# Kernel tuning notes

Hardware: AMD Instinct MI355X
Metric: run time of the kernel (lower is better)

The kernel has to match this reference:

```python
import jax, jax.numpy as jnp
import numpy as np
import math

B, S, D = 2, 2048, 2048
H, KV = 16, 4
HD = D // H          # 128
REP = H // KV        # 4


def setup_inputs() -> dict:
    key = jax.random.key(0)
    ks = jax.random.split(key, 6)
    x = jax.random.normal(ks[0], (B, S, D), dtype=jnp.float32)
    wq = jax.random.normal(ks[1], (D, D), dtype=jnp.float32) * (D ** -0.5)
    wk = jax.random.normal(ks[2], (KV * HD, D), dtype=jnp.float32) * (D ** -0.5)
    wv = jax.random.normal(ks[3], (KV * HD, D), dtype=jnp.float32) * (D ** -0.5)
    wo = jax.random.normal(ks[4], (D, D), dtype=jnp.float32) * (D ** -0.5)
    # RoPE frequencies: theta_i = 10000^(-2i/hd), angle = pos * theta_i
    inv_freq = 1.0 / (10000.0 ** (np.arange(0, HD, 2, dtype=np.float32) / HD))
    angles = np.arange(S, dtype=np.float32)[:, None] * inv_freq[None, :]  # [S, HD/2]
    freqs_cos = jnp.asarray(np.cos(angles), dtype=jnp.float32)
    freqs_sin = jnp.asarray(np.sin(angles), dtype=jnp.float32)
    return {"x": x, "wq": wq, "wk": wk, "wv": wv, "wo": wo,
            "freqs_cos": freqs_cos, "freqs_sin": freqs_sin}


def _rope(t, cos, sin):
    # t: [B, S, h, HD]; cos/sin: [S, HD/2]; complex multiply on (even, odd) pairs
    tr = t.reshape(*t.shape[:-1], HD // 2, 2)
    t0, t1 = tr[..., 0], tr[..., 1]
    c = cos[None, :, None, :]
    s = sin[None, :, None, :]
    o0 = t0 * c - t1 * s
    o1 = t0 * s + t1 * c
    return jnp.stack([o0, o1], axis=-1).reshape(t.shape)


def reference(x, wq, wk, wv, wo, freqs_cos, freqs_sin):
    # projections (torch Linear: y = x @ W.T)
    q = jnp.einsum('bsd,ed->bse', x, wq).reshape(B, S, H, HD)
    k = jnp.einsum('bsd,ed->bse', x, wk).reshape(B, S, KV, HD)
    v = jnp.einsum('bsd,ed->bse', x, wv).reshape(B, S, KV, HD)
    q = _rope(q, freqs_cos, freqs_sin)
    k = _rope(k, freqs_cos, freqs_sin)
    # GQA: repeat each kv head REP times -> [B, S, H, HD]
    k = jnp.repeat(k, REP, axis=2)
    v = jnp.repeat(v, REP, axis=2)
    # [B, H, S, HD]
    q = q.transpose(0, 2, 1, 3)
    k = k.transpose(0, 2, 1, 3)
    v = v.transpose(0, 2, 1, 3)
    scores = jnp.einsum('bhqd,bhkd->bhqk', q, k) * (1.0 / math.sqrt(HD))
    # faithful to torch: tril then masked_fill(scores == 0, -inf)
    scores = jnp.tril(scores)
    scores = jnp.where(scores == 0.0, -jnp.inf, scores)
    attn = jax.nn.softmax(scores, axis=-1)
    out = jnp.einsum('bhqk,bhkd->bhqd', attn, v)
    out = out.transpose(0, 2, 1, 3).reshape(B, S, D)
    return jnp.einsum('bsd,ed->bse', out, wo)
```

## Files before the change

kernel.cpp:

```cpp
#include <hip/hip_runtime.h>
#include <stdint.h>

#define B_ 2
#define S_ 2048
#define D_ 2048
#define NH 16
#define NKV 4
#define HD_ 128

typedef unsigned short u16;
typedef unsigned int u32;
typedef __attribute__((ext_vector_type(8))) __bf16 bf16x8;
typedef __attribute__((ext_vector_type(4))) float f32x4;
typedef __attribute__((ext_vector_type(16))) float f32x16;
typedef __attribute__((ext_vector_type(4))) unsigned int u32x4;
typedef __attribute__((ext_vector_type(8))) unsigned short ushort8v;

__device__ __forceinline__ u16 f2bf(float f) {
  u32 u = __builtin_bit_cast(u32, f);
  u32 r = (u + 0x7FFFu + ((u >> 16) & 1u)) >> 16;
  return (u16)r;
}
__device__ __forceinline__ float bf2f(u16 h) {
  return __builtin_bit_cast(float, ((u32)h) << 16);
}
__device__ __forceinline__ u32 cvtpk(float lo, float hi) {
  u32 r;
  asm("v_cvt_pk_bf16_f32 %0, %1, %2" : "=v"(r) : "v"(lo), "v"(hi));
  return r;
}
__device__ __forceinline__ f32x16 zero16() {
  f32x16 v;
#pragma unroll
  for (int i = 0; i < 16; ++i) v[i] = 0.f;
  return v;
}

__device__ __forceinline__ void gld_lds16(const void* g, void* l) {
  __builtin_amdgcn_global_load_lds(
      (const __attribute__((address_space(1))) void*)g,
      (__attribute__((address_space(3))) void*)l, 16, 0, 0);
}

__device__ __forceinline__ void cv8(const float* s, u16* d, int i) {
  const float4* sp = (const float4*)s + 2 * (size_t)i;
  float4 a = sp[0], b = sp[1];
  ushort8v o;
  o[0] = f2bf(a.x); o[1] = f2bf(a.y); o[2] = f2bf(a.z); o[3] = f2bf(a.w);
  o[4] = f2bf(b.x); o[5] = f2bf(b.y); o[6] = f2bf(b.z); o[7] = f2bf(b.w);
  *((ushort8v*)d + i) = o;
}
__global__ __launch_bounds__(256) void k_f2b_all(const float* __restrict__ x,
    const float* __restrict__ wq, const float* __restrict__ wk,
    const float* __restrict__ wv, const float* __restrict__ wo,
    u16* __restrict__ xb, u16* __restrict__ wqkv, u16* __restrict__ wob) {
  int i = blockIdx.x * 256 + threadIdx.x;
  if (i < 1048576) { cv8(x, xb, i); return; }
  i -= 1048576;
  if (i < 524288) { cv8(wq, wqkv, i); return; }
  i -= 524288;
  if (i < 131072) { cv8(wk, wqkv + 2048 * 2048, i); return; }
  i -= 131072;
  if (i < 131072) { cv8(wv, wqkv + 2560 * 2048, i); return; }
  i -= 131072;
  if (i < 524288) cv8(wo, wob, i);
}

__global__ __launch_bounds__(256) void k_gemm_bf(const u16* __restrict__ A,
    const u16* __restrict__ W, u16* __restrict__ C, int N, int K) {
  __shared__ char lds[32768];
  char* ldsA = lds;
  char* ldsB = lds + 16384;
  const int tid = threadIdx.x;
  const int lane = tid & 63;
  const int wave = tid >> 6;
  const int m0 = blockIdx.x * 128, n0 = blockIdx.y * 128;
  const int wm = (wave >> 1) * 64, wn = (wave & 1) * 64;
  f32x4 acc[4][4];
#pragma unroll
  for (int i = 0; i < 4; ++i)
#pragma unroll
    for (int j = 0; j < 4; ++j) acc[i][j] = f32x4{0.f, 0.f, 0.f, 0.f};
  const size_t Kb2 = (size_t)K * 2;
  int rowS[4], colS[4];
#pragma unroll
  for (int j = 0; j < 4; ++j) {
    int plin = j * 4096 + tid * 16;
    int o = plin ^ (((plin >> 7) & 7) << 4);
    rowS[j] = o >> 7;
    colS[j] = o & 127;
  }
  for (int kt = 0; kt < K; kt += 64) {
#pragma unroll
    for (int j = 0; j < 4; ++j) {
      gld_lds16((const char*)A + (size_t)(m0 + rowS[j]) * Kb2 + (size_t)kt * 2 + colS[j],
                ldsA + j * 4096 + wave * 1024);
      gld_lds16((const char*)W + (size_t)(n0 + rowS[j]) * Kb2 + (size_t)kt * 2 + colS[j],
                ldsB + j * 4096 + wave * 1024);
    }
    __syncthreads();
#pragma unroll
    for (int kk = 0; kk < 2; ++kk) {
      const int colb = kk * 64 + ((lane >> 4) << 4);
      bf16x8 af[4], bfv[4];
#pragma unroll
      for (int mi = 0; mi < 4; ++mi) {
        int row = wm + mi * 16 + (lane & 15);
        af[mi] = *(const bf16x8*)(ldsA + (row << 7) + (colb ^ ((row & 7) << 4)));
      }
#pragma unroll
      for (int ni = 0; ni < 4; ++ni) {
        int row = wn + ni * 16 + (lane & 15);
        bfv[ni] = *(const bf16x8*)(ldsB + (row << 7) + (colb ^ ((row & 7) << 4)));
      }
#pragma unroll
      for (int mi = 0; mi < 4; ++mi)
#pragma unroll
        for (int ni = 0; ni < 4; ++ni)
          acc[mi][ni] = __builtin_amdgcn_mfma_f32_16x16x32_bf16(af[mi], bfv[ni], acc[mi][ni], 0, 0, 0);
    }
    __syncthreads();
  }
#pragma unroll
  for (int mi = 0; mi < 4; ++mi)
#pragma unroll
    for (int ni = 0; ni < 4; ++ni) {
      const int n = n0 + wn + ni * 16 + (lane & 15);
#pragma unroll
      for (int r = 0; r < 4; ++r) {
        const int m = m0 + wm + mi * 16 + ((lane >> 4) << 2) + r;
        C[(size_t)m * N + n] = f2bf(acc[mi][ni][r]);
      }
    }
}

__global__ __launch_bounds__(512, 1) void k_gemm_out(const u16* __restrict__ A,
    const u16* __restrict__ W, float* __restrict__ C, int N, int K) {
  __shared__ char lds[2][49152];
  const int tid = threadIdx.x, lane = tid & 63, wave = tid >> 6;
  const int wm = wave >> 2, wn = wave & 3;
  const int m0 = blockIdx.x * 256, n0 = blockIdx.y * 128;
  const size_t Kb2 = (size_t)K * 2;
  f32x4 acc[8][2];
#pragma unroll
  for (int mi = 0; mi < 8; ++mi)
#pragma unroll
    for (int ni = 0; ni < 2; ++ni) acc[mi][ni] = f32x4{0.f, 0.f, 0.f, 0.f};
  int rA[4], cA[4], rB[2], cB[2];
#pragma unroll
  for (int j = 0; j < 4; ++j) {
    int p = j * 8192 + tid * 16;
    int o = p ^ (((p >> 7) & 7) << 4);
    rA[j] = o >> 7; cA[j] = o & 127;
  }
#pragma unroll
  for (int j = 0; j < 2; ++j) {
    int p = j * 8192 + tid * 16;
    int o = p ^ (((p >> 7) & 7) << 4);
    rB[j] = o >> 7; cB[j] = o & 127;
  }
  auto stage = [&](int t) {
    char* dst = &lds[t & 1][0];
    const char* As = (const char*)A + (size_t)t * 128;
    const char* Ws = (const char*)W + (size_t)t * 128;
#pragma unroll
    for (int j = 0; j < 4; ++j)
      gld_lds16(As + (size_t)(m0 + rA[j]) * Kb2 + cA[j], dst + j * 8192 + tid * 16);
#pragma unroll
    for (int j = 0; j < 2; ++j)
      gld_lds16(Ws + (size_t)(n0 + rB[j]) * Kb2 + cB[j], dst + 32768 + j * 8192 + tid * 16);
  };
  stage(0);
  __syncthreads();
  const int nt = K >> 6;
  for (int t = 0; t < nt; ++t) {
    if (t + 1 < nt) stage(t + 1);
    const char* buf = &lds[t & 1][0];
#pragma unroll
    for (int kk = 0; kk < 2; ++kk) {
      const int cb = kk * 64 + ((lane >> 4) << 4);
      bf16x8 af[8], bfr[2];
#pragma unroll
      for (int mi = 0; mi < 8; ++mi) {
        int r = wm * 128 + mi * 16 + (lane & 15);
        af[mi] = *(const bf16x8*)(buf + (r << 7) + (cb ^ ((r & 7) << 4)));
      }
#pragma unroll
      for (int ni = 0; ni < 2; ++ni) {
        int r = wn * 32 + ni * 16 + (lane & 15);
        bfr[ni] = *(const bf16x8*)(buf + 32768 + (r << 7) + (cb ^ ((r & 7) << 4)));
      }
      __builtin_amdgcn_s_setprio(1);
#pragma unroll
      for (int mi = 0; mi < 8; ++mi)
#pragma unroll
        for (int ni = 0; ni < 2; ++ni)
          acc[mi][ni] = __builtin_amdgcn_mfma_f32_16x16x32_bf16(af[mi], bfr[ni], acc[mi][ni], 0, 0, 0);
      __builtin_amdgcn_s_setprio(0);
    }
    __syncthreads();
  }
#pragma unroll
  for (int mi = 0; mi < 8; ++mi)
#pragma unroll
    for (int ni = 0; ni < 2; ++ni) {
      const int n = n0 + wn * 32 + ni * 16 + (lane & 15);
#pragma unroll
      for (int r = 0; r < 4; ++r) {
        const int m = m0 + wm * 128 + mi * 16 + ((lane >> 4) << 2) + r;
        C[(size_t)m * N + n] = acc[mi][ni][r];
      }
    }
}

__device__ __forceinline__ void rope_one(const u16* __restrict__ src,
    u16* __restrict__ dst, const float* __restrict__ fc, const float* __restrict__ fs,
    int nh, int lognh, int dorope, int idx, int coloff, float smul) {
  const int q4 = idx & 15;
  const int rest = idx >> 4;
  const int hidx = rest & (nh - 1);
  const int t = rest >> lognh;
  const int b = t >> 11, s = t & 2047;
  ushort8v ev = *(const ushort8v*)(src + (size_t)t * 3072 + coloff + hidx * HD_ + q4 * 8);
  float e[8];
#pragma unroll
  for (int j = 0; j < 8; ++j) e[j] = bf2f(ev[j]);
  float o[8];
  if (dorope) {
    float4 c4 = *(const float4*)(fc + s * 64 + q4 * 4);
    float4 s4 = *(const float4*)(fs + s * 64 + q4 * 4);
    float cc[4] = {c4.x, c4.y, c4.z, c4.w};
    float ss[4] = {s4.x, s4.y, s4.z, s4.w};
#pragma unroll
    for (int j = 0; j < 4; ++j) {
      o[2 * j]     = (e[2 * j] * cc[j] - e[2 * j + 1] * ss[j]) * smul;
      o[2 * j + 1] = (e[2 * j] * ss[j] + e[2 * j + 1] * cc[j]) * smul;
    }
  } else {
#pragma unroll
    for (int j = 0; j < 8; ++j) o[j] = e[j] * smul;
  }
  ushort8v w;
#pragma unroll
  for (int j = 0; j < 8; ++j) w[j] = f2bf(o[j]);
  *(ushort8v*)(dst + (((size_t)(b * nh + hidx)) * S_ + s) * HD_ + q4 * 8) = w;
}
__global__ __launch_bounds__(256) void k_rope_all(const u16* __restrict__ src,
    u16* __restrict__ Qd, u16* __restrict__ Kd, u16* __restrict__ Vd,
    const float* __restrict__ fc, const float* __restrict__ fs) {
  const float QS = 0.08838834764831845f * 1.4426950408889634f;
  int i = blockIdx.x * 256 + threadIdx.x;
  if (i < 1048576) { rope_one(src, Qd, fc, fs, 16, 4, 1, i, 0, QS); return; }
  i -= 1048576;
  if (i < 262144) { rope_one(src, Kd, fc, fs, 4, 2, 1, i, 2048, 1.0f); return; }
  i -= 262144;
  rope_one(src, Vd, fc, fs, 4, 2, 0, i, 2560, 1.0f);
}

__global__ __launch_bounds__(256, 2) void k_attn(const u16* __restrict__ Q,
    const u16* __restrict__ Kt, const u16* __restrict__ Vt, u16* __restrict__ O) {
  __shared__ char kls[2][16384];
  __shared__ char vls[2][16384];
  const int h = blockIdx.x, b = blockIdx.y;
  const int z = blockIdx.z;
  const int qtb = (z < 8) ? (15 - z) : (z - 8);
  const int tid = threadIdx.x, lane = tid & 63, wave = tid >> 6;
  const int ql = lane & 31, g = lane >> 5;
  const int kvh = h >> 2;
  const u16* Qb = Q + ((size_t)(b * NH + h)) * S_ * HD_;
  const u16* Kb = Kt + ((size_t)(b * NKV + kvh)) * S_ * HD_;
  const u16* Vb = Vt + ((size_t)(b * NKV + kvh)) * S_ * HD_;
  const int q0 = qtb * 128, qw0 = q0 + wave * 32;
  const int qme = qw0 + ql;
  int kRowS[4], kColS[4];
#pragma unroll
  for (int j = 0; j < 4; ++j) {
    int plin = j * 4096 + tid * 16;
    int o = plin ^ (((plin >> 8) & 7) << 4);
    kRowS[j] = o >> 8;
    kColS[j] = o & 255;
  }
  const int kp = tid & 31, hb = (tid >> 5) * 16;
  auto loadV = [&](int tn, u32* vr0, u32* vr1) {
    const u16* vp = Vb + (size_t)(tn * 64 + 2 * kp) * HD_ + hb;
    const u32* r0 = (const u32*)vp;
    const u32* r1 = (const u32*)(vp + HD_);
#pragma unroll
    for (int wd = 0; wd < 8; ++wd) { vr0[wd] = r0[wd]; vr1[wd] = r1[wd]; }
  };
  auto writeV = [&](char* vn, const u32* vr0, const u32* vr1) {
#pragma unroll
    for (int wd = 0; wd < 8; ++wd) {
      u32 v0 = vr0[wd], v1 = vr1[wd];
      u32 lo = (v0 & 0xFFFFu) | (v1 << 16);
      u32 hi = (v0 >> 16) | (v1 & 0xFFFF0000u);
      int hd0 = hb + 2 * wd, hd1 = hd0 + 1;
      *(u32*)(vn + hd0 * 128 + ((4 * kp) ^ ((hd0 & 7) << 4))) = lo;
      *(u32*)(vn + hd1 * 128 + ((4 * kp) ^ ((hd1 & 7) << 4))) = hi;
    }
  };

#pragma unroll
  for (int j = 0; j < 4; ++j)
    gld_lds16((const char*)Kb + (size_t)kRowS[j] * 256 + kColS[j],
              &kls[0][0] + j * 4096 + wave * 1024);
  u32 pv0[8], pv1[8];
  loadV(0, pv0, pv1);
  bf16x8 qf[8];
#pragma unroll
  for (int kk = 0; kk < 8; ++kk)
    qf[kk] = *(const bf16x8*)(Qb + (size_t)qme * HD_ + kk * 16 + g * 8);
  writeV(&vls[0][0], pv0, pv1);
  __syncthreads();

  f32x16 oacc[4];
#pragma unroll
  for (int th = 0; th < 4; ++th) oacc[th] = zero16();
  float mrun = -1e30f, lrun = 0.0f;
  const int nt = 2 * qtb + 2;

  int cur = 0;
  for (int t = 0; t < nt; ++t) {
    const int kv0 = t * 64;
    const bool haveNext = (t + 1 < nt);
    u32 vr0[8], vr1[8];
    if (haveNext) {
      const int kvn = kv0 + 64;
#pragma unroll
      for (int j = 0; j < 4; ++j)
        gld_lds16((const char*)Kb + (size_t)(kvn + kRowS[j]) * 256 + kColS[j],
                  &kls[cur ^ 1][0] + j * 4096 + wave * 1024);
      loadV(t + 1, vr0, vr1);
    }
    if (kv0 <= qw0 + 31) {
      const char* kcur = &kls[cur][0];
      const char* vcur = &vls[cur][0];
      f32x16 c0 = zero16(), c1 = zero16();
      __builtin_amdgcn_s_setprio(1);
#pragma unroll
      for (int kk = 0; kk < 8; ++kk) {
        const int sw = (kk * 32 + 16 * g) ^ ((ql & 7) << 4);
        bf16x8 kf0 = *(const bf16x8*)(kcur + (ql << 8) + sw);
        bf16x8 kf1 = *(const bf16x8*)(kcur + ((32 + ql) << 8) + sw);
        c0 = __builtin_amdgcn_mfma_f32_32x32x16_bf16(kf0, qf[kk], c0, 0, 0, 0);
        c1 = __builtin_amdgcn_mfma_f32_32x32x16_bf16(kf1, qf[kk], c1, 0, 0, 0);
      }
      __builtin_amdgcn_s_setprio(0);
      const bool diag = (kv0 + 63 > qw0);
      float mt = -1e30f;
      if (diag) {
#pragma unroll
        for (int r = 0; r < 16; ++r) {
          float s0 = c0[r], s1 = c1[r];
          int kb = kv0 + (r & 3) + ((r >> 2) << 3) + 4 * g;
          if (kb > qme) s0 = -1e30f;
          if (kb + 32 > qme) s1 = -1e30f;
          c0[r] = s0; c1[r] = s1;
          mt = fmaxf(mt, fmaxf(s0, s1));
        }
      } else {
#pragma unroll
        for (int r = 0; r < 16; ++r)
          mt = fmaxf(mt, fmaxf(c0[r], c1[r]));
      }
      mt = fmaxf(mt, __shfl_xor(mt, 32));
      if (!__all(mt <= mrun + 8.0f)) {
        float mnew = fmaxf(mrun, mt);
        float alpha = exp2f(mrun - mnew);
        lrun *= alpha;
        mrun = mnew;
#pragma unroll
        for (int r = 0; r < 16; ++r) {
          float av = __shfl(alpha, 36 * g + (r & 3) + ((r >> 2) << 3));
          oacc[0][r] *= av; oacc[1][r] *= av;
          oacc[2][r] *= av; oacc[3][r] *= av;
        }
      }
      float lt = 0.0f;
#pragma unroll
      for (int r = 0; r < 16; ++r) {
        float p0 = exp2f(c0[r] - mrun);
        float p1 = exp2f(c1[r] - mrun);
        c0[r] = p0; c1[r] = p1;
        lt += p0 + p1;
      }
      lt += __shfl_xor(lt, 32);
      lrun += lt;
      u32 paw[4][4];
#pragma unroll
      for (int a = 0; a < 2; ++a) {
        {
          u32 X = cvtpk(c0[8 * a + 0], c0[8 * a + 1]);
          u32 Y = cvtpk(c0[8 * a + 2], c0[8 * a + 3]);
          u32 Z = cvtpk(c0[8 * a + 4], c0[8 * a + 5]);
          u32 W = cvtpk(c0[8 * a + 6], c0[8 * a + 7]);
          u32 S1 = g ? X : Z, S2 = g ? Y : W;
          u32 R1 = (u32)__shfl_xor((int)S1, 32), R2 = (u32)__shfl_xor((int)S2, 32);
          paw[a][0] = g ? R1 : X; paw[a][1] = g ? R2 : Y;
          paw[a][2] = g ? Z : R1; paw[a][3] = g ? W : R2;
        }
        {
          u32 X = cvtpk(c1[8 * a + 0], c1[8 * a + 1]);
          u32 Y = cvtpk(c1[8 * a + 2], c1[8 * a + 3]);
          u32 Z = cvtpk(c1[8 * a + 4], c1[8 * a + 5]);
          u32 W = cvtpk(c1[8 * a + 6], c1[8 * a + 7]);
          u32 S1 = g ? X : Z, S2 = g ? Y : W;
          u32 R1 = (u32)__shfl_xor((int)S1, 32), R2 = (u32)__shfl_xor((int)S2, 32);
          paw[2 + a][0] = g ? R1 : X; paw[2 + a][1] = g ? R2 : Y;
          paw[2 + a][2] = g ? Z : R1; paw[2 + a][3] = g ? W : R2;
        }
      }
      __builtin_amdgcn_s_setprio(1);
#pragma unroll
      for (int ks = 0; ks < 4; ++ks) {
        bf16x8 pf = __builtin_bit_cast(bf16x8,
            u32x4{paw[ks][0], paw[ks][1], paw[ks][2], paw[ks][3]});
        const int cb = (32 * ks + 16 * g) ^ ((ql & 7) << 4);
#pragma unroll
        for (int th = 0; th < 4; ++th) {
          bf16x8 vf = *(const bf16x8*)(vcur + ((th * 32 + ql) << 7) + cb);
          oacc[th] = __builtin_amdgcn_mfma_f32_32x32x16_bf16(pf, vf, oacc[th], 0, 0, 0);
        }
      }
      __builtin_amdgcn_s_setprio(0);
    }
    if (haveNext) writeV(&vls[cur ^ 1][0], vr0, vr1);
    __syncthreads();
    cur ^= 1;
  }
#pragma unroll
  for (int r = 0; r < 16; ++r) {
    float lr = __shfl(lrun, 36 * g + (r & 3) + ((r >> 2) << 3));
    float li = 1.0f / lr;
    int q = qw0 + (r & 3) + ((r >> 2) << 3) + 4 * g;
    size_t rowo = (size_t)(b * S_ + q) * D_ + h * HD_ + ql;
#pragma unroll
    for (int th = 0; th < 4; ++th)
      O[rowo + 32 * th] = f2bf(oacc[th][r] * li);
  }
}

extern "C" void kernel_launch(void* const* d_in, const int* in_sizes, int n_in,
                              void* d_out, int out_size, void* d_ws, size_t ws_size,
                              hipStream_t stream) {
  const float* x  = (const float*)d_in[0];
  const float* wq = (const float*)d_in[1];
  const float* wk = (const float*)d_in[2];
  const float* wv = (const float*)d_in[3];
  const float* wo = (const float*)d_in[4];
  const float* fc = (const float*)d_in[5];
  const float* fs = (const float*)d_in[6];
  float* out = (float*)d_out;
  char* ws = (char*)d_ws;
  const size_t MB = 1ull << 20;
  u16* xb    = (u16*)(ws);
  u16* wqkv  = (u16*)(ws + 16 * MB);
  u16* wob   = (u16*)(ws + 28 * MB);
  u16* qkvbf = (u16*)(ws + 36 * MB);
  u16* Qb    = (u16*)(ws);
  u16* Kb    = (u16*)(ws + 16 * MB);
  u16* Vb    = (u16*)(ws + 20 * MB);
  u16* attb  = (u16*)(ws + 36 * MB);

  k_f2b_all<<<dim3(9216), dim3(256), 0, stream>>>(x, wq, wk, wv, wo, xb, wqkv, wob);

  k_gemm_bf<<<dim3(32, 24), dim3(256), 0, stream>>>(xb, wqkv, qkvbf, 3072, D_);

  k_rope_all<<<dim3(6144), dim3(256), 0, stream>>>(qkvbf, Qb, Kb, Vb, fc, fs);

  k_attn<<<dim3(NH, B_, 16), dim3(256), 0, stream>>>(Qb, Kb, Vb, attb);

  k_gemm_out<<<dim3(16, 16), dim3(512), 0, stream>>>(attb, wob, out, D_, D_);
}
```

Measured before the change: 217.7 us.

## Fuse RoPE, scaling and head-major scatter into QKV GEMM epilogue; use raw v_exp

Removes the separate RoPE kernel by applying rotary embedding, the Q scale and the head-major relayout directly in the QKV projection GEMM epilogue, using a lane shuffle to fetch the paired element. This drops one kernel launch and a full write and read of the intermediate QKV buffer. In exchange the epilogue now does scalar, poorly coalesced bf16 stores and per-element cos/sin loads. Separately, the attention softmax swaps exp2f for the raw v_exp_f32 instruction to avoid the library's range handling.

```diff
diff --git a/kernel.cpp b/kernel.cpp
--- a/kernel.cpp
+++ b/kernel.cpp
@@ -29,6 +29,11 @@
   asm("v_cvt_pk_bf16_f32 %0, %1, %2" : "=v"(r) : "v"(lo), "v"(hi));
   return r;
 }
+__device__ __forceinline__ float fexp2(float x) {
+  float r;
+  asm("v_exp_f32 %0, %1" : "=v"(r) : "v"(x));
+  return r;
+}
 __device__ __forceinline__ f32x16 zero16() {
   f32x16 v;
 #pragma unroll
@@ -41,6 +46,8 @@
       (const __attribute__((address_space(1))) void*)g,
       (__attribute__((address_space(3))) void*)l, 16, 0, 0);
 }
+
+#define QSCALE 0.12750527540095196f
 
 __device__ __forceinline__ void cv8(const float* s, u16* d, int i) {
   const float4* sp = (const float4*)s + 2 * (size_t)i;
@@ -66,8 +73,10 @@
   if (i < 524288) cv8(wo, wob, i);
 }
 
-__global__ __launch_bounds__(256) void k_gemm_bf(const u16* __restrict__ A,
-    const u16* __restrict__ W, u16* __restrict__ C, int N, int K) {
+__global__ __launch_bounds__(256) void k_gemm_qkv(const u16* __restrict__ A,
+    const u16* __restrict__ W, u16* __restrict__ Qd, u16* __restrict__ Kd,
+    u16* __restrict__ Vd, const float* __restrict__ fc,
+    const float* __restrict__ fs, int K) {
   __shared__ char lds[32768];
   char* ldsA = lds;
   char* ldsB = lds + 16384;
@@ -121,17 +130,47 @@
     }
     __syncthreads();
   }
-#pragma unroll
-  for (int mi = 0; mi < 4; ++mi)
+  const int seg = blockIdx.y;
+  const int bb = m0 >> 11;
+  if (seg < 20) {
+    const bool isQ = (seg < 16);
+    const int h = isQ ? seg : seg - 16;
+    u16* dstB = isQ ? (Qd + ((size_t)(bb * NH + h)) * S_ * HD_)
+                    : (Kd + ((size_t)(bb * NKV + h)) * S_ * HD_);
+    const float sc = isQ ? QSCALE : 1.0f;
 #pragma unroll
     for (int ni = 0; ni < 4; ++ni) {
-      const int n = n0 + wn + ni * 16 + (lane & 15);
-#pragma unroll
-      for (int r = 0; r < 4; ++r) {
-        const int m = m0 + wm + mi * 16 + ((lane >> 4) << 2) + r;
-        C[(size_t)m * N + n] = f2bf(acc[mi][ni][r]);
-      }
-    }
+      const int c = wn + ni * 16 + (lane & 15);
+      const int j = c >> 1;
+#pragma unroll
+      for (int mi = 0; mi < 4; ++mi)
+#pragma unroll
+        for (int r = 0; r < 4; ++r) {
+          const int m = m0 + wm + mi * 16 + ((lane >> 4) << 2) + r;
+          const int s = m & 2047;
+          float val = acc[mi][ni][r];
+          float par = __shfl_xor(val, 1);
+          float cs = fc[s * 64 + j], sn = fs[s * 64 + j];
+          float outv = (c & 1) ? (par * sn + val * cs) : (val * cs - par * sn);
+          dstB[(size_t)s * HD_ + c] = f2bf(outv * sc);
+        }
+    }
+  } else {
+    const int h = seg - 20;
+    u16* dstB = Vd + ((size_t)(bb * NKV + h)) * S_ * HD_;
+#pragma unroll
+    for (int ni = 0; ni < 4; ++ni) {
+      const int c = wn + ni * 16 + (lane & 15);
+#pragma unroll
+      for (int mi = 0; mi < 4; ++mi)
+#pragma unroll
+        for (int r = 0; r < 4; ++r) {
+          const int m = m0 + wm + mi * 16 + ((lane >> 4) << 2) + r;
+          const int s = m & 2047;
+          dstB[(size_t)s * HD_ + c] = f2bf(acc[mi][ni][r]);
+        }
+    }
+  }
 }
 
 __global__ __launch_bounds__(512, 1) void k_gemm_out(const u16* __restrict__ A,
@@ -211,50 +250,6 @@
         C[(size_t)m * N + n] = acc[mi][ni][r];
       }
     }
-}
-
-__device__ __forceinline__ void rope_one(const u16* __restrict__ src,
-    u16* __restrict__ dst, const float* __restrict__ fc, const float* __restrict__ fs,
-    int nh, int lognh, int dorope, int idx, int coloff, float smul) {
-  const int q4 = idx & 15;
-  const int rest = idx >> 4;
-  const int hidx = rest & (nh - 1);
-  const int t = rest >> lognh;
-  const int b = t >> 11, s = t & 2047;
-  ushort8v ev = *(const ushort8v*)(src + (size_t)t * 3072 + coloff + hidx * HD_ + q4 * 8);
-  float e[8];
-#pragma unroll
-  for (int j = 0; j < 8; ++j) e[j] = bf2f(ev[j]);
-  float o[8];
-  if (dorope) {
-    float4 c4 = *(const float4*)(fc + s * 64 + q4 * 4);
-    float4 s4 = *(const float4*)(fs + s * 64 + q4 * 4);
-    float cc[4] = {c4.x, c4.y, c4.z, c4.w};
-    float ss[4] = {s4.x, s4.y, s4.z, s4.w};
-#pragma unroll
-    for (int j = 0; j < 4; ++j) {
-      o[2 * j]     = (e[2 * j] * cc[j] - e[2 * j + 1] * ss[j]) * smul;
-      o[2 * j + 1] = (e[2 * j] * ss[j] + e[2 * j + 1] * cc[j]) * smul;
-    }
-  } else {
-#pragma unroll
-    for (int j = 0; j < 8; ++j) o[j] = e[j] * smul;
-  }
-  ushort8v w;
-#pragma unroll
-  for (int j = 0; j < 8; ++j) w[j] = f2bf(o[j]);
-  *(ushort8v*)(dst + (((size_t)(b * nh + hidx)) * S_ + s) * HD_ + q4 * 8) = w;
-}
-__global__ __launch_bounds__(256) void k_rope_all(const u16* __restrict__ src,
-    u16* __restrict__ Qd, u16* __restrict__ Kd, u16* __restrict__ Vd,
-    const float* __restrict__ fc, const float* __restrict__ fs) {
-  const float QS = 0.08838834764831845f * 1.4426950408889634f;
-  int i = blockIdx.x * 256 + threadIdx.x;
-  if (i < 1048576) { rope_one(src, Qd, fc, fs, 16, 4, 1, i, 0, QS); return; }
-  i -= 1048576;
-  if (i < 262144) { rope_one(src, Kd, fc, fs, 4, 2, 1, i, 2048, 1.0f); return; }
-  i -= 262144;
-  rope_one(src, Vd, fc, fs, 4, 2, 0, i, 2560, 1.0f);
 }
 
 __global__ __launch_bounds__(256, 2) void k_attn(const u16* __restrict__ Q,
@@ -366,7 +361,7 @@
       mt = fmaxf(mt, __shfl_xor(mt, 32));
       if (!__all(mt <= mrun + 8.0f)) {
         float mnew = fmaxf(mrun, mt);
-        float alpha = exp2f(mrun - mnew);
+        float alpha = fexp2(mrun - mnew);
         lrun *= alpha;
         mrun = mnew;
 #pragma unroll
@@ -379,8 +374,8 @@
       float lt = 0.0f;
 #pragma unroll
       for (int r = 0; r < 16; ++r) {
-        float p0 = exp2f(c0[r] - mrun);
-        float p1 = exp2f(c1[r] - mrun);
+        float p0 = fexp2(c0[r] - mrun);
+        float p1 = fexp2(c1[r] - mrun);
         c0[r] = p0; c1[r] = p1;
         lt += p0 + p1;
       }
@@ -453,20 +448,17 @@
   float* out = (float*)d_out;
   char* ws = (char*)d_ws;
   const size_t MB = 1ull << 20;
-  u16* xb    = (u16*)(ws);
-  u16* wqkv  = (u16*)(ws + 16 * MB);
-  u16* wob   = (u16*)(ws + 28 * MB);
-  u16* qkvbf = (u16*)(ws + 36 * MB);
-  u16* Qb    = (u16*)(ws);
-  u16* Kb    = (u16*)(ws + 16 * MB);
-  u16* Vb    = (u16*)(ws + 20 * MB);
-  u16* attb  = (u16*)(ws + 36 * MB);
+  u16* xb   = (u16*)(ws);
+  u16* wqkv = (u16*)(ws + 16 * MB);
+  u16* wob  = (u16*)(ws + 28 * MB);
+  u16* Qb   = (u16*)(ws + 36 * MB);
+  u16* Kb   = (u16*)(ws + 52 * MB);
+  u16* Vb   = (u16*)(ws + 56 * MB);
+  u16* attb = (u16*)(ws);
 
   k_f2b_all<<<dim3(9216), dim3(256), 0, stream>>>(x, wq, wk, wv, wo, xb, wqkv, wob);
 
-  k_gemm_bf<<<dim3(32, 24), dim3(256), 0, stream>>>(xb, wqkv, qkvbf, 3072, D_);
-
-  k_rope_all<<<dim3(6144), dim3(256), 0, stream>>>(qkvbf, Qb, Kb, Vb, fc, fs);
+  k_gemm_qkv<<<dim3(32, 24), dim3(256), 0, stream>>>(xb, wqkv, Qb, Kb, Vb, fc, fs, D_);
 
   k_attn<<<dim3(NH, B_, 16), dim3(256), 0, stream>>>(Qb, Kb, Vb, attb);
 
```

New measurement: 218.1 us. Within noise of the previous version (+0.2%).
